# Kernel tuning notes

Measured on AMD Instinct MI355X. Metric: run time of the kernel, lower is better.

The kernel has to match this reference:

```python
import jax, jax.numpy as jnp
import numpy as np

B, S, D, H = 2, 4096, 1024, 16
DK = D // H


def setup_inputs() -> dict:
    key = jax.random.key(0)
    ks = jax.random.split(key, 7)
    sc = 1.0 / np.sqrt(D)
    return {
        "q": jax.random.normal(ks[0], (B, S, D), jnp.float32),
        "k": jax.random.normal(ks[1], (B, S, D), jnp.float32),
        "v": jax.random.normal(ks[2], (B, S, D), jnp.float32),
        "wq": jax.random.normal(ks[3], (D, D), jnp.float32) * sc,
        "wk": jax.random.normal(ks[4], (D, D), jnp.float32) * sc,
        "wv": jax.random.normal(ks[5], (D, D), jnp.float32) * sc,
        "w0": jax.random.normal(ks[6], (D, D), jnp.float32) * sc,
    }


def reference(q, k, v, wq, wk, wv, w0):
    # Linear(bias=False): y = x @ W^T  (torch convention, W is [out,in])
    qp = jnp.einsum('bsd,ed->bse', q, wq).reshape(B, S, H, DK).transpose(0, 2, 1, 3)
    kp = jnp.einsum('bsd,ed->bse', k, wk).reshape(B, S, H, DK).transpose(0, 2, 1, 3)
    vp = jnp.einsum('bsd,ed->bse', v, wv).reshape(B, S, H, DK).transpose(0, 2, 1, 3)
    scale = 1.0 / jnp.sqrt(jnp.float32(DK))
    att = jnp.einsum('bhqd,bhkd->bhqk', qp, kp) * scale  # [B,H,S,S]
    att = jax.nn.softmax(att, axis=-1)
    x = jnp.einsum('bhqk,bhkd->bhqd', att, vp)  # [B,H,S,DK]
    x = x.transpose(0, 2, 1, 3).reshape(B, S, D)
    out = jnp.einsum('bsd,ed->bse', x, w0)
    return out
```

## Files before the change

kernel.cpp:

```cpp
#include <hip/hip_runtime.h>
#include <hip/hip_bf16.h>
#include <stdint.h>

#define Bb 2
#define Ss 4096
#define Dd 1024
#define Hh 16
#define DKk 64

typedef __attribute__((ext_vector_type(8))) short bf16x8;
typedef __attribute__((ext_vector_type(4))) float f32x4;
typedef __attribute__((ext_vector_type(16))) float f32x16;

#define MFMA16(a, b, c) __builtin_amdgcn_mfma_f32_32x32x16_bf16(a, b, c, 0, 0, 0)

__device__ __forceinline__ unsigned short f2bf(float f) {
    union { float f; unsigned int u; } x; x.f = f;
    return (unsigned short)((x.u + 0x7fffu + ((x.u >> 16) & 1u)) >> 16);
}

__device__ __forceinline__ void gload16(const void* g, void* l) {
    __builtin_amdgcn_global_load_lds(
        (const __attribute__((address_space(1))) void*)g,
        (__attribute__((address_space(3))) void*)l, 16, 0, 0);
}

__device__ __forceinline__ float max3f(float a, float b, float c) {
    return fmaxf(fmaxf(a, b), c);
}

__global__ __launch_bounds__(256) void cvt_all(const float* __restrict__ q, const float* __restrict__ k,
                                               const float* __restrict__ v, const float* __restrict__ wq,
                                               const float* __restrict__ wk, const float* __restrict__ wv,
                                               const float* __restrict__ w0, unsigned short* __restrict__ ws) {
    const int QKV4 = 3 * 2097152;
    const int TOT4 = QKV4 + 4 * 262144;
    int i = blockIdx.x * 256 + threadIdx.x;
    const int stride = gridDim.x * 256;
    ushort4* out = (ushort4*)ws;
    for (; i < TOT4; i += stride) {
        const float4* src;
        int di;
        if (i < QKV4) {
            const int r = i >> 21;
            const float* s = r == 0 ? q : (r == 1 ? k : v);
            src = (const float4*)s + (i & 2097151);
            di = i;
        } else {
            const int j = i - QKV4;
            const int r = j >> 18;
            const float* s = r == 0 ? wq : (r == 1 ? wk : (r == 2 ? wv : w0));
            src = (const float4*)s + (j & 262143);
            di = i + 2097152;
        }
        const float4 vv = *src;
        ushort4 o;
        o.x = f2bf(vv.x); o.y = f2bf(vv.y); o.z = f2bf(vv.z); o.w = f2bf(vv.w);
        out[di] = o;
    }
}

template <int MODE>
__global__ __launch_bounds__(256) void gemm_bt(const unsigned short* __restrict__ A,
                                               const unsigned short* __restrict__ W,
                                               void* __restrict__ Y) {
    __shared__ unsigned short As[128 * 32];
    __shared__ unsigned short Bs[128 * 32];
    const int t = threadIdx.x;
    const int wid = t >> 6, lane = t & 63, q4 = lane >> 4, l16 = lane & 15;
    const int wr = wid >> 1, wc = wid & 1;
    const int arow0 = blockIdx.x * 128;
    const int wrow0 = blockIdx.y * 128;
    f32x4 acc[4][4] = {};
    for (int kt = 0; kt < 1024; kt += 32) {
        __syncthreads();
#pragma unroll
        for (int i = 0; i < 2; i++) {
            const int o = i * 4096 + t * 16;
            const int r = o >> 6, c = (o & 63) >> 1;
            gload16(A + (long)(arow0 + r) * 1024 + kt + c, (char*)As + o);
            gload16(W + (long)(wrow0 + r) * 1024 + kt + c, (char*)Bs + o);
        }
        __syncthreads();
        bf16x8 a[4], b[4];
#pragma unroll
        for (int m = 0; m < 4; m++)
            a[m] = *(const bf16x8*)((const char*)As + (wr * 64 + m * 16 + l16) * 64 + q4 * 16);
#pragma unroll
        for (int n = 0; n < 4; n++)
            b[n] = *(const bf16x8*)((const char*)Bs + (wc * 64 + n * 16 + l16) * 64 + q4 * 16);
#pragma unroll
        for (int m = 0; m < 4; m++)
#pragma unroll
            for (int n = 0; n < 4; n++)
                acc[m][n] = __builtin_amdgcn_mfma_f32_16x16x32_bf16(a[m], b[n], acc[m][n], 0, 0, 0);
    }
    const int rb = arow0 + wr * 64, cb = wrow0 + wc * 64;
#pragma unroll
    for (int m = 0; m < 4; m++)
#pragma unroll
        for (int n = 0; n < 4; n++)
#pragma unroll
            for (int r = 0; r < 4; r++) {
                const int row = rb + m * 16 + q4 * 4 + r;
                const int col = cb + n * 16 + l16;
                const float v = acc[m][n][r];
                if (MODE == 0) {
                    ((unsigned short*)Y)[(long)row * 1024 + col] = f2bf(v);
                } else if (MODE == 1) {
                    const int bb = row >> 12, s = row & 4095;
                    const int hh = col >> 6, dk = col & 63;
                    ((unsigned short*)Y)[(((long)(bb * Hh + hh) * DKk + dk) << 12) + s] = f2bf(v);
                } else {
                    ((float*)Y)[(long)row * 1024 + col] = v;
                }
            }
}

__global__ __launch_bounds__(256, 4) void attn_fwd(const unsigned short* __restrict__ qp,
                                                   const unsigned short* __restrict__ kp,
                                                   const unsigned short* __restrict__ vt,
                                                   unsigned short* __restrict__ xo) {
    __shared__ __align__(16) char smem[32768];
    const int t = threadIdx.x;
    const int wid = t >> 6, lane = t & 63;
    const int l5 = lane & 31;
    const int ihi = lane >> 5;
    const int e5 = l5 & 7;
    const int qt = blockIdx.x, h = blockIdx.y, b = blockIdx.z;
    const unsigned short* qbase = qp + ((long)b * Ss + qt * 128) * Dd + h * 64;
    const unsigned short* kbase = kp + (long)b * Ss * Dd + h * 64;
    const unsigned short* vbase = vt + (long)(b * Hh + h) * DKk * Ss;
    char* Qs = smem + 16384;

#pragma unroll
    for (int i = 0; i < 4; i++) {
        const int o = i * 4096 + t * 16;
        const int r = o >> 7;
        const int c = ((o & 127) ^ ((r & 7) << 4)) >> 1;
        gload16(qbase + (long)r * Dd + c, Qs + o);
    }
    const int o0 = t * 16;
    const int r0 = o0 >> 7;
    const int c0 = ((o0 & 127) ^ ((r0 & 7) << 4)) >> 1;
    const unsigned short* ksrc = kbase + (long)r0 * Dd + c0;
    const unsigned short* vsrc = vbase + (long)r0 * Ss + c0;
    gload16(ksrc,             smem + o0);
    gload16(ksrc + 32 * Dd,   smem + 4096 + o0);
    gload16(vsrc,             smem + 8192 + o0);
    gload16(vsrc + 32 * Ss,   smem + 12288 + o0);
    asm volatile("s_waitcnt vmcnt(4)" ::: "memory");
    __builtin_amdgcn_s_barrier();
    asm volatile("" ::: "memory");

    const int qrow = wid * 32 + l5;
    bf16x8 bQ[4];
#pragma unroll
    for (int m = 0; m < 4; m++) {
        const int slot = (m * 2 + ihi) ^ (qrow & 7);
        bQ[m] = *(const bf16x8*)(Qs + qrow * 128 + (slot << 4));
    }
    asm volatile("s_waitcnt lgkmcnt(0)" ::: "memory");
    __builtin_amdgcn_s_barrier();
    asm volatile("" ::: "memory");
    gload16(ksrc + 64 * Dd,        smem + 16384 + o0);
    gload16(ksrc + 96 * Dd,        smem + 20480 + o0);
    gload16(vsrc + 64,             smem + 24576 + o0);
    gload16(vsrc + 32 * Ss + 64,   smem + 28672 + o0);
    const unsigned short* pk = ksrc + 128 * Dd;
    const unsigned short* pv = vsrc + 128;
    asm volatile("s_waitcnt vmcnt(4)" ::: "memory");
    __builtin_amdgcn_s_barrier();
    asm volatile("" ::: "memory");

    int adm[4];
#pragma unroll
    for (int m = 0; m < 4; m++)
        adm[m] = l5 * 128 + ((((m * 2 + ihi) ^ e5)) << 4);

    const float c1f = 0.1803368801111244f;
    float mi = -1e30f, li = 0.f;
    f32x16 accO[2] = {};

    for (int kt2 = 0; kt2 < 64; kt2 += 2) {
#pragma unroll
        for (int hf = 0; hf < 2; hf++) {
            const int kt = kt2 + hf;
            const int BO = hf << 14;
            const char* Kc = smem + BO;
            const char* Vc = smem + BO + 8192;
            f32x16 accS[2] = {};
            __builtin_amdgcn_s_setprio(1);
#pragma unroll
            for (int m = 0; m < 4; m++) {
                const bf16x8 aK0 = *(const bf16x8*)(Kc + adm[m]);
                const bf16x8 aK1 = *(const bf16x8*)(Kc + 4096 + adm[m]);
                accS[0] = MFMA16(aK0, bQ[m], accS[0]);
                accS[1] = MFMA16(aK1, bQ[m], accS[1]);
            }
            __builtin_amdgcn_s_setprio(0);
            float m0 = max3f(accS[0][0], accS[0][1], accS[0][2]);
            m0 = max3f(m0, accS[0][3], accS[0][4]);
            m0 = max3f(m0, accS[0][5], accS[0][6]);
            m0 = fmaxf(m0, accS[0][7]);
            float m1 = max3f(accS[0][8], accS[0][9], accS[0][10]);
            m1 = max3f(m1, accS[0][11], accS[0][12]);
            m1 = max3f(m1, accS[0][13], accS[0][14]);
            m1 = fmaxf(m1, accS[0][15]);
            float m2 = max3f(accS[1][0], accS[1][1], accS[1][2]);
            m2 = max3f(m2, accS[1][3], accS[1][4]);
            m2 = max3f(m2, accS[1][5], accS[1][6]);
            m2 = fmaxf(m2, accS[1][7]);
            float m3 = max3f(accS[1][8], accS[1][9], accS[1][10]);
            m3 = max3f(m3, accS[1][11], accS[1][12]);
            m3 = max3f(m3, accS[1][13], accS[1][14]);
            m3 = fmaxf(m3, accS[1][15]);
            const float rmx = fmaxf(max3f(m0, m1, m2), m3);
            if (!__all(rmx * c1f <= mi + 8.f)) {
                const float r2 = fmaxf(rmx, __shfl_xor(rmx, 32, 64));
                const float mn = fmaxf(mi, r2 * c1f);
                const float alpha = __builtin_amdgcn_exp2f(mi - mn);
                mi = mn;
                li *= alpha;
#pragma unroll
                for (int d = 0; d < 2; d++)
#pragma unroll
                    for (int r = 0; r < 16; r++) accO[d][r] *= alpha;
            }
            unsigned pwu[2][4][2];
            float psa[4] = {0.f, 0.f, 0.f, 0.f};
#pragma unroll
            for (int kb = 0; kb < 2; kb++)
#pragma unroll
                for (int s = 0; s < 4; s++)
#pragma unroll
                    for (int w = 0; w < 2; w++) {
                        const float p0 = __builtin_amdgcn_exp2f(fmaf(accS[kb][4 * s + 2 * w],     c1f, -mi));
                        const float p1 = __builtin_amdgcn_exp2f(fmaf(accS[kb][4 * s + 2 * w + 1], c1f, -mi));
                        psa[kb * 2 + w] += p0 + p1;
                        asm("v_cvt_pk_bf16_f32 %0, %1, %2" : "=v"(pwu[kb][s][w]) : "v"(p0), "v"(p1));
                    }
            float ps = (psa[0] + psa[1]) + (psa[2] + psa[3]);
            ps += __shfl_xor(ps, 32, 64);
            li += ps;
            __builtin_amdgcn_s_setprio(1);
#pragma unroll
            for (int m = 0; m < 4; m++) {
                const int kb = m >> 1, s0 = (m & 1) * 2;
                unsigned x0 = pwu[kb][s0][0], y0 = pwu[kb][s0 + 1][0];
                unsigned x1 = pwu[kb][s0][1], y1 = pwu[kb][s0 + 1][1];
                asm("v_permlane32_swap_b32 %0, %1" : "+v"(x0), "+v"(y0));
                asm("v_permlane32_swap_b32 %0, %1" : "+v"(x1), "+v"(y1));
                union { unsigned u[4]; bf16x8 v; } fr;
                fr.u[0] = x0; fr.u[1] = x1; fr.u[2] = y0; fr.u[3] = y1;
#pragma unroll
                for (int dblk = 0; dblk < 2; dblk++) {
                    const bf16x8 aV = *(const bf16x8*)(Vc + dblk * 4096 + adm[m]);
                    accO[dblk] = MFMA16(aV, fr.v, accO[dblk]);
                }
            }
            __builtin_amdgcn_s_setprio(0);
            __builtin_amdgcn_s_barrier();
            asm volatile("" ::: "memory");
            if (kt < 62) {
                char* dst = smem + BO;
                gload16(pk,            dst + o0);
                gload16(pk + 32 * Dd,  dst + 4096 + o0);
                gload16(pv,            dst + 8192 + o0);
                gload16(pv + 32 * Ss,  dst + 12288 + o0);
                pk += 64 * Dd;
                pv += 64;
                asm volatile("s_waitcnt vmcnt(4)" ::: "memory");
            } else {
                asm volatile("s_waitcnt vmcnt(0)" ::: "memory");
            }
            __builtin_amdgcn_s_barrier();
            asm volatile("" ::: "memory");
        }
    }

    const float rli = 1.0f / li;
    const int erow = wid * 32 + l5;
#pragma unroll
    for (int dblk = 0; dblk < 2; dblk++)
#pragma unroll
        for (int tt = 0; tt < 8; tt++) {
            const unsigned short b0 = f2bf(accO[dblk][2 * tt] * rli);
            const unsigned short b1 = f2bf(accO[dblk][2 * tt + 1] * rli);
            const int slot = (dblk * 4 + (tt >> 1)) ^ e5;
            const int phys = erow * 128 + (slot << 4) + ihi * 8 + (tt & 1) * 4;
            *(unsigned*)(smem + phys) = ((unsigned)b1 << 16) | b0;
        }
    __syncthreads();
#pragma unroll
    for (int p = 0; p < 4; p++) {
        const int o = p * 4096 + t * 16;
        const int row = o >> 7;
        const int slot = (o & 127) >> 4;
        const uint4 val = *(const uint4*)(smem + row * 128 + ((slot ^ (row & 7)) << 4));
        *(uint4*)((char*)(xo + ((long)b * Ss + qt * 128 + row) * Dd + h * 64) + slot * 16) = val;
    }
}

extern "C" void kernel_launch(void* const* d_in, const int* in_sizes, int n_in,
                              void* d_out, int out_size, void* d_ws, size_t ws_size,
                              hipStream_t stream) {
    const float* q  = (const float*)d_in[0];
    const float* k  = (const float*)d_in[1];
    const float* v  = (const float*)d_in[2];
    const float* wq = (const float*)d_in[3];
    const float* wk = (const float*)d_in[4];
    const float* wv = (const float*)d_in[5];
    const float* w0 = (const float*)d_in[6];

    unsigned short* ws = (unsigned short*)d_ws;
    const long NE = (long)Bb * Ss * Dd;
    unsigned short* qb  = ws;
    unsigned short* kb  = ws + NE;
    unsigned short* vb  = ws + 2 * NE;
    unsigned short* x1  = ws + 3 * NE;
    unsigned short* wqb = ws + 4 * NE;
    unsigned short* wkb = wqb + 1048576;
    unsigned short* wvb = wkb + 1048576;
    unsigned short* w0b = wvb + 1048576;

    cvt_all<<<2048, 256, 0, stream>>>(q, k, v, wq, wk, wv, w0, ws);

    dim3 gg(64, 8);
    gemm_bt<0><<<gg, 256, 0, stream>>>(qb, wqb, x1);
    gemm_bt<0><<<gg, 256, 0, stream>>>(kb, wkb, qb);
    gemm_bt<1><<<gg, 256, 0, stream>>>(vb, wvb, kb);
    dim3 ga(32, 16, 2);
    attn_fwd<<<ga, 256, 0, stream>>>(x1, qb, kb, vb);
    gemm_bt<2><<<gg, 256, 0, stream>>>(vb, w0b, (float*)d_out);
}
```

Measured before the change: 304.8 us.

## Process two 32-row query blocks per warp to double K/V tile reuse

Each attention block now handles 256 query rows instead of 128, and each warp keeps two Q fragments with separate softmax state, so every K/V tile loaded into LDS and every K/V fragment read from LDS feeds twice as many MFMAs. The LDS swizzle also gains an extra XOR term to reduce bank conflicts. The grid is halved and launch bounds drop to 2 blocks per CU, which raises register pressure and lowers occupancy and block count, reducing parallelism across CUs.

```diff
diff --git a/kernel.cpp b/kernel.cpp
--- a/kernel.cpp
+++ b/kernel.cpp
@@ -117,7 +117,7 @@
             }
 }
 
-__global__ __launch_bounds__(256, 4) void attn_fwd(const unsigned short* __restrict__ qp,
+__global__ __launch_bounds__(256, 2) void attn_fwd(const unsigned short* __restrict__ qp,
                                                    const unsigned short* __restrict__ kp,
                                                    const unsigned short* __restrict__ vt,
                                                    unsigned short* __restrict__ xo) {
@@ -126,43 +126,44 @@
     const int wid = t >> 6, lane = t & 63;
     const int l5 = lane & 31;
     const int ihi = lane >> 5;
-    const int e5 = l5 & 7;
+    const int swz5 = (l5 & 7) ^ ((l5 >> 3) & 3);
     const int qt = blockIdx.x, h = blockIdx.y, b = blockIdx.z;
-    const unsigned short* qbase = qp + ((long)b * Ss + qt * 128) * Dd + h * 64;
+    const unsigned short* qbase = qp + ((long)b * Ss + qt * 256) * Dd + h * 64;
     const unsigned short* kbase = kp + (long)b * Ss * Dd + h * 64;
     const unsigned short* vbase = vt + (long)(b * Hh + h) * DKk * Ss;
-    char* Qs = smem + 16384;
-
-#pragma unroll
-    for (int i = 0; i < 4; i++) {
-        const int o = i * 4096 + t * 16;
-        const int r = o >> 7;
-        const int c = ((o & 127) ^ ((r & 7) << 4)) >> 1;
-        gload16(qbase + (long)r * Dd + c, Qs + o);
-    }
+
+    const int r0 = t >> 3;
+    const int s0 = t & 7;
+    const int cb0 = s0 ^ (r0 & 7) ^ ((r0 >> 3) & 3);
     const int o0 = t * 16;
-    const int r0 = o0 >> 7;
-    const int c0 = ((o0 & 127) ^ ((r0 & 7) << 4)) >> 1;
-    const unsigned short* ksrc = kbase + (long)r0 * Dd + c0;
-    const unsigned short* vsrc = vbase + (long)r0 * Ss + c0;
-    gload16(ksrc,             smem + o0);
-    gload16(ksrc + 32 * Dd,   smem + 4096 + o0);
-    gload16(vsrc,             smem + 8192 + o0);
-    gload16(vsrc + 32 * Ss,   smem + 12288 + o0);
-    asm volatile("s_waitcnt vmcnt(4)" ::: "memory");
+    const unsigned short* qsrc = qbase + (long)r0 * Dd + cb0 * 8;
+    const unsigned short* ksrc = kbase + (long)r0 * Dd + cb0 * 8;
+    const unsigned short* vsrc = vbase + (long)r0 * Ss + cb0 * 8;
+
+#pragma unroll
+    for (int i = 0; i < 8; i++)
+        gload16(qsrc + (long)i * 32 * Dd, smem + i * 4096 + o0);
+    asm volatile("s_waitcnt vmcnt(0)" ::: "memory");
     __builtin_amdgcn_s_barrier();
     asm volatile("" ::: "memory");
 
-    const int qrow = wid * 32 + l5;
-    bf16x8 bQ[4];
-#pragma unroll
-    for (int m = 0; m < 4; m++) {
-        const int slot = (m * 2 + ihi) ^ (qrow & 7);
-        bQ[m] = *(const bf16x8*)(Qs + qrow * 128 + (slot << 4));
-    }
+    bf16x8 bQ[2][4];
+#pragma unroll
+    for (int qb = 0; qb < 2; qb++)
+#pragma unroll
+        for (int m = 0; m < 4; m++) {
+            const int chunk = wid * 2 + qb;
+            const int slot = (m * 2 + ihi) ^ swz5;
+            bQ[qb][m] = *(const bf16x8*)(smem + chunk * 4096 + l5 * 128 + (slot << 4));
+        }
     asm volatile("s_waitcnt lgkmcnt(0)" ::: "memory");
     __builtin_amdgcn_s_barrier();
     asm volatile("" ::: "memory");
+
+    gload16(ksrc,                  smem + o0);
+    gload16(ksrc + 32 * Dd,        smem + 4096 + o0);
+    gload16(vsrc,                  smem + 8192 + o0);
+    gload16(vsrc + 32 * Ss,        smem + 12288 + o0);
     gload16(ksrc + 64 * Dd,        smem + 16384 + o0);
     gload16(ksrc + 96 * Dd,        smem + 20480 + o0);
     gload16(vsrc + 64,             smem + 24576 + o0);
@@ -176,11 +177,11 @@
     int adm[4];
 #pragma unroll
     for (int m = 0; m < 4; m++)
-        adm[m] = l5 * 128 + ((((m * 2 + ihi) ^ e5)) << 4);
+        adm[m] = l5 * 128 + ((((m * 2 + ihi) ^ swz5)) << 4);
 
     const float c1f = 0.1803368801111244f;
-    float mi = -1e30f, li = 0.f;
-    f32x16 accO[2] = {};
+    float mi[2] = {-1e30f, -1e30f}, li[2] = {0.f, 0.f};
+    f32x16 accO[2][2] = {};
 
     for (int kt2 = 0; kt2 < 64; kt2 += 2) {
 #pragma unroll
@@ -189,74 +190,81 @@
             const int BO = hf << 14;
             const char* Kc = smem + BO;
             const char* Vc = smem + BO + 8192;
-            f32x16 accS[2] = {};
+            f32x16 accS[2][2] = {};
             __builtin_amdgcn_s_setprio(1);
 #pragma unroll
             for (int m = 0; m < 4; m++) {
                 const bf16x8 aK0 = *(const bf16x8*)(Kc + adm[m]);
                 const bf16x8 aK1 = *(const bf16x8*)(Kc + 4096 + adm[m]);
-                accS[0] = MFMA16(aK0, bQ[m], accS[0]);
-                accS[1] = MFMA16(aK1, bQ[m], accS[1]);
+                accS[0][0] = MFMA16(aK0, bQ[0][m], accS[0][0]);
+                accS[0][1] = MFMA16(aK1, bQ[0][m], accS[0][1]);
+                accS[1][0] = MFMA16(aK0, bQ[1][m], accS[1][0]);
+                accS[1][1] = MFMA16(aK1, bQ[1][m], accS[1][1]);
             }
             __builtin_amdgcn_s_setprio(0);
-            float m0 = max3f(accS[0][0], accS[0][1], accS[0][2]);
-            m0 = max3f(m0, accS[0][3], accS[0][4]);
-            m0 = max3f(m0, accS[0][5], accS[0][6]);
-            m0 = fmaxf(m0, accS[0][7]);
-            float m1 = max3f(accS[0][8], accS[0][9], accS[0][10]);
-            m1 = max3f(m1, accS[0][11], accS[0][12]);
-            m1 = max3f(m1, accS[0][13], accS[0][14]);
-            m1 = fmaxf(m1, accS[0][15]);
-            float m2 = max3f(accS[1][0], accS[1][1], accS[1][2]);
-            m2 = max3f(m2, accS[1][3], accS[1][4]);
-            m2 = max3f(m2, accS[1][5], accS[1][6]);
-            m2 = fmaxf(m2, accS[1][7]);
-            float m3 = max3f(accS[1][8], accS[1][9], accS[1][10]);
-            m3 = max3f(m3, accS[1][11], accS[1][12]);
-            m3 = max3f(m3, accS[1][13], accS[1][14]);
-            m3 = fmaxf(m3, accS[1][15]);
-            const float rmx = fmaxf(max3f(m0, m1, m2), m3);
-            if (!__all(rmx * c1f <= mi + 8.f)) {
-                const float r2 = fmaxf(rmx, __shfl_xor(rmx, 32, 64));
-                const float mn = fmaxf(mi, r2 * c1f);
-                const float alpha = __builtin_amdgcn_exp2f(mi - mn);
-                mi = mn;
-                li *= alpha;
-#pragma unroll
-                for (int d = 0; d < 2; d++)
-#pragma unroll
-                    for (int r = 0; r < 16; r++) accO[d][r] *= alpha;
-            }
-            unsigned pwu[2][4][2];
-            float psa[4] = {0.f, 0.f, 0.f, 0.f};
-#pragma unroll
-            for (int kb = 0; kb < 2; kb++)
-#pragma unroll
-                for (int s = 0; s < 4; s++)
-#pragma unroll
-                    for (int w = 0; w < 2; w++) {
-                        const float p0 = __builtin_amdgcn_exp2f(fmaf(accS[kb][4 * s + 2 * w],     c1f, -mi));
-                        const float p1 = __builtin_amdgcn_exp2f(fmaf(accS[kb][4 * s + 2 * w + 1], c1f, -mi));
-                        psa[kb * 2 + w] += p0 + p1;
-                        asm("v_cvt_pk_bf16_f32 %0, %1, %2" : "=v"(pwu[kb][s][w]) : "v"(p0), "v"(p1));
-                    }
-            float ps = (psa[0] + psa[1]) + (psa[2] + psa[3]);
-            ps += __shfl_xor(ps, 32, 64);
-            li += ps;
+            unsigned pwu[2][2][4][2];
+#pragma unroll
+            for (int qb = 0; qb < 2; qb++) {
+                float m0 = max3f(accS[qb][0][0], accS[qb][0][1], accS[qb][0][2]);
+                m0 = max3f(m0, accS[qb][0][3], accS[qb][0][4]);
+                m0 = max3f(m0, accS[qb][0][5], accS[qb][0][6]);
+                m0 = fmaxf(m0, accS[qb][0][7]);
+                float m1 = max3f(accS[qb][0][8], accS[qb][0][9], accS[qb][0][10]);
+                m1 = max3f(m1, accS[qb][0][11], accS[qb][0][12]);
+                m1 = max3f(m1, accS[qb][0][13], accS[qb][0][14]);
+                m1 = fmaxf(m1, accS[qb][0][15]);
+                float m2 = max3f(accS[qb][1][0], accS[qb][1][1], accS[qb][1][2]);
+                m2 = max3f(m2, accS[qb][1][3], accS[qb][1][4]);
+                m2 = max3f(m2, accS[qb][1][5], accS[qb][1][6]);
+                m2 = fmaxf(m2, accS[qb][1][7]);
+                float m3 = max3f(accS[qb][1][8], accS[qb][1][9], accS[qb][1][10]);
+                m3 = max3f(m3, accS[qb][1][11], accS[qb][1][12]);
+                m3 = max3f(m3, accS[qb][1][13], accS[qb][1][14]);
+                m3 = fmaxf(m3, accS[qb][1][15]);
+                const float rmx = fmaxf(max3f(m0, m1, m2), m3);
+                if (!__all(rmx * c1f <= mi[qb] + 8.f)) {
+                    const float r2 = fmaxf(rmx, __shfl_xor(rmx, 32, 64));
+                    const float mn = fmaxf(mi[qb], r2 * c1f);
+                    const float alpha = __builtin_amdgcn_exp2f(mi[qb] - mn);
+                    mi[qb] = mn;
+                    li[qb] *= alpha;
+#pragma unroll
+                    for (int d = 0; d < 2; d++)
+#pragma unroll
+                        for (int r = 0; r < 16; r++) accO[d][qb][r] *= alpha;
+                }
+                float psa[4] = {0.f, 0.f, 0.f, 0.f};
+#pragma unroll
+                for (int kb = 0; kb < 2; kb++)
+#pragma unroll
+                    for (int s = 0; s < 4; s++)
+#pragma unroll
+                        for (int w = 0; w < 2; w++) {
+                            const float p0 = __builtin_amdgcn_exp2f(fmaf(accS[qb][kb][4 * s + 2 * w],     c1f, -mi[qb]));
+                            const float p1 = __builtin_amdgcn_exp2f(fmaf(accS[qb][kb][4 * s + 2 * w + 1], c1f, -mi[qb]));
+                            psa[kb * 2 + w] += p0 + p1;
+                            asm("v_cvt_pk_bf16_f32 %0, %1, %2" : "=v"(pwu[qb][kb][s][w]) : "v"(p0), "v"(p1));
+                        }
+                float ps = (psa[0] + psa[1]) + (psa[2] + psa[3]);
+                ps += __shfl_xor(ps, 32, 64);
+                li[qb] += ps;
+            }
             __builtin_amdgcn_s_setprio(1);
 #pragma unroll
             for (int m = 0; m < 4; m++) {
-                const int kb = m >> 1, s0 = (m & 1) * 2;
-                unsigned x0 = pwu[kb][s0][0], y0 = pwu[kb][s0 + 1][0];
-                unsigned x1 = pwu[kb][s0][1], y1 = pwu[kb][s0 + 1][1];
-                asm("v_permlane32_swap_b32 %0, %1" : "+v"(x0), "+v"(y0));
-                asm("v_permlane32_swap_b32 %0, %1" : "+v"(x1), "+v"(y1));
-                union { unsigned u[4]; bf16x8 v; } fr;
-                fr.u[0] = x0; fr.u[1] = x1; fr.u[2] = y0; fr.u[3] = y1;
-#pragma unroll
-                for (int dblk = 0; dblk < 2; dblk++) {
-                    const bf16x8 aV = *(const bf16x8*)(Vc + dblk * 4096 + adm[m]);
-                    accO[dblk] = MFMA16(aV, fr.v, accO[dblk]);
+                const bf16x8 aV0 = *(const bf16x8*)(Vc + adm[m]);
+                const bf16x8 aV1 = *(const bf16x8*)(Vc + 4096 + adm[m]);
+                const int kb = m >> 1, sx = (m & 1) * 2;
+#pragma unroll
+                for (int qb = 0; qb < 2; qb++) {
+                    unsigned x0 = pwu[qb][kb][sx][0], y0 = pwu[qb][kb][sx + 1][0];
+                    unsigned x1 = pwu[qb][kb][sx][1], y1 = pwu[qb][kb][sx + 1][1];
+                    asm("v_permlane32_swap_b32 %0, %1" : "+v"(x0), "+v"(y0));
+                    asm("v_permlane32_swap_b32 %0, %1" : "+v"(x1), "+v"(y1));
+                    union { unsigned u[4]; bf16x8 v; } fr;
+                    fr.u[0] = x0; fr.u[1] = x1; fr.u[2] = y0; fr.u[3] = y1;
+                    accO[0][qb] = MFMA16(aV0, fr.v, accO[0][qb]);
+                    accO[1][qb] = MFMA16(aV1, fr.v, accO[1][qb]);
                 }
             }
             __builtin_amdgcn_s_setprio(0);
@@ -279,26 +287,27 @@
         }
     }
 
-    const float rli = 1.0f / li;
-    const int erow = wid * 32 + l5;
-#pragma unroll
-    for (int dblk = 0; dblk < 2; dblk++)
-#pragma unroll
-        for (int tt = 0; tt < 8; tt++) {
-            const unsigned short b0 = f2bf(accO[dblk][2 * tt] * rli);
-            const unsigned short b1 = f2bf(accO[dblk][2 * tt + 1] * rli);
-            const int slot = (dblk * 4 + (tt >> 1)) ^ e5;
-            const int phys = erow * 128 + (slot << 4) + ihi * 8 + (tt & 1) * 4;
-            *(unsigned*)(smem + phys) = ((unsigned)b1 << 16) | b0;
-        }
+#pragma unroll
+    for (int qb = 0; qb < 2; qb++) {
+        const float rli = 1.0f / li[qb];
+        const int chunk = wid * 2 + qb;
+#pragma unroll
+        for (int dblk = 0; dblk < 2; dblk++)
+#pragma unroll
+            for (int tt = 0; tt < 8; tt++) {
+                const unsigned short b0 = f2bf(accO[dblk][qb][2 * tt] * rli);
+                const unsigned short b1 = f2bf(accO[dblk][qb][2 * tt + 1] * rli);
+                const int slot = (dblk * 4 + (tt >> 1)) ^ swz5;
+                const int phys = chunk * 4096 + l5 * 128 + (slot << 4) + ihi * 8 + (tt & 1) * 4;
+                *(unsigned*)(smem + phys) = ((unsigned)b1 << 16) | b0;
+            }
+    }
     __syncthreads();
 #pragma unroll
-    for (int p = 0; p < 4; p++) {
-        const int o = p * 4096 + t * 16;
-        const int row = o >> 7;
-        const int slot = (o & 127) >> 4;
-        const uint4 val = *(const uint4*)(smem + row * 128 + ((slot ^ (row & 7)) << 4));
-        *(uint4*)((char*)(xo + ((long)b * Ss + qt * 128 + row) * Dd + h * 64) + slot * 16) = val;
+    for (int p = 0; p < 8; p++) {
+        const uint4 val = *(const uint4*)(smem + p * 4096 + o0);
+        const long row = (long)qt * 256 + p * 32 + r0;
+        *(uint4*)(xo + ((long)b * Ss + row) * Dd + h * 64 + cb0 * 8) = val;
     }
 }
 
@@ -330,7 +339,7 @@
     gemm_bt<0><<<gg, 256, 0, stream>>>(qb, wqb, x1);
     gemm_bt<0><<<gg, 256, 0, stream>>>(kb, wkb, qb);
     gemm_bt<1><<<gg, 256, 0, stream>>>(vb, wvb, kb);
-    dim3 ga(32, 16, 2);
+    dim3 ga(16, 16, 2);
     attn_fwd<<<ga, 256, 0, stream>>>(x1, qb, kb, vb);
     gemm_bt<2><<<gg, 256, 0, stream>>>(vb, w0b, (float*)d_out);
 }
```

Result: faster. 285.2 us (-6.4%).
